# Performance work log

Measured on AMD Instinct MI355X. Metric: run time of the kernel, lower is better.

## Reference

```python
import jax, jax.numpy as jnp
import numpy as np

T, B, D_IN, H, N_OUT = 512, 256, 85, 512, 33

def setup_inputs() -> dict:
    key = jax.random.key(0)
    ks = jax.random.split(key, 16)
    s_in = 1.0 / np.sqrt(D_IN)
    s_h = 1.0 / np.sqrt(H)
    def u(k, shape, s):
        return jax.random.uniform(k, shape, jnp.float32, -s, s)
    return {
        "x": jax.random.normal(ks[0], (T, B, D_IN), jnp.float32),
        "Wxi": u(ks[1], (H, D_IN), s_in),
        "Wxf": u(ks[2], (H, D_IN), s_in),
        "Wxo": u(ks[3], (H, D_IN), s_in),
        "Wxc": u(ks[4], (H, D_IN), s_in),
        "Whi": u(ks[5], (H, H), s_h), "bhi": u(ks[6], (H,), s_h),
        "Whf": u(ks[7], (H, H), s_h), "bhf": u(ks[8], (H,), s_h),
        "Who": u(ks[9], (H, H), s_h), "bho": u(ks[10], (H,), s_h),
        "Whc": u(ks[11], (H, H), s_h), "bhc": u(ks[12], (H,), s_h),
        "Wro": u(ks[13], (N_OUT, H), s_h), "bro": u(ks[14], (N_OUT,), s_h),
    }

def _lstm(x, Wxi, Wxf, Wxo, Wxc, Whi, bhi, Whf, bhf, Who, bho, Whc, bhc, Wro, bro):
    act = jnp.tanh  # hp['activation'] == 'tanh'
    # Precompute all input-side projections in one big GEMM-like pass: [T,B,H]
    xi = jnp.einsum('tbi,hi->tbh', x, Wxi)
    xf = jnp.einsum('tbi,hi->tbh', x, Wxf)
    xo = jnp.einsum('tbi,hi->tbh', x, Wxo)
    xc = jnp.einsum('tbi,hi->tbh', x, Wxc)
    Bsz = x.shape[1]
    Hd = Whi.shape[0]
    C0 = jnp.zeros((Bsz, Hd), x.dtype)
    H0 = jnp.zeros((Bsz, Hd), x.dtype)

    def step(carry, xs):
        C, Hs = carry
        xi_t, xf_t, xo_t, xc_t = xs
        I = jax.nn.sigmoid(xi_t + Hs @ Whi.T + bhi)
        F = jax.nn.sigmoid(xf_t + Hs @ Whf.T + bhf)
        O = jax.nn.sigmoid(xo_t + Hs @ Who.T + bho)
        C_hat = act(xc_t + Hs @ Whc.T + bhc)
        C = F * C + I * C_hat
        Hs = O * act(C)
        return (C, Hs), Hs

    _, hidden_states = jax.lax.scan(step, (C0, H0), (xi, xf, xo, xc))
    # readout over all timesteps: [T,B,n_output]
    return jnp.einsum('tbh,oh->tbo', hidden_states, Wro) + bro

def reference(x, Wxi, Wxf, Wxo, Wxc, Whi, bhi, Whf, bhf, Who, bho, Whc, bhc, Wro, bro):
    return _lstm(x, Wxi, Wxf, Wxo, Wxc, Whi, bhi, Whf, bhf, Who, bho, Whc, bhc, Wro, bro)
```

## Files before the change

### kernel.cpp

```cpp
#include <hip/hip_runtime.h>
#include <hip/hip_bf16.h>
#include <stdint.h>

#define T_STEPS 512
#define BATCH   256
#define DIN     85
#define HDIM    512
#define NOUT    33

#define GRP   16
#define BBLK  16
#define HS    32
#define LDA   1040
#define LDX   208

#define SENT  0x7FC07FC0u

typedef __attribute__((ext_vector_type(8))) short s8v;
typedef __attribute__((ext_vector_type(4))) float f4v;
typedef __attribute__((ext_vector_type(4))) uint32_t u32x4;

__device__ __forceinline__ uint16_t f2bf(float f) {
    uint32_t x = __builtin_bit_cast(uint32_t, f);
    uint32_t r = (x + 0x7fffu + ((x >> 16) & 1u)) >> 16;
    return (uint16_t)r;
}
__device__ __forceinline__ float sigm(float v) {
    v = fminf(fmaxf(v, -30.f), 30.f);
    return 1.f / (1.f + __expf(-v));
}
__device__ __forceinline__ float tanh_f(float v) {
    v = fminf(fmaxf(v, -15.f), 15.f);
    float e = __expf(2.f * v);
    return (e - 1.f) / (e + 1.f);
}
__device__ __forceinline__ s8v cvt8(const float* p) {
    s8v v;
#pragma unroll
    for (int j = 0; j < 8; ++j) v[j] = (short)f2bf(p[j]);
    return v;
}

__device__ __forceinline__ void issue4(u32x4& v, const uint32_t* p) {
    asm volatile("global_load_dwordx4 %0, %1, off sc0 sc1"
                 : "+v"(v) : "v"(p) : "memory");
}
__device__ __forceinline__ void wait_vm1(u32x4& a, u32x4& b, u32x4& c, u32x4& d) {
    asm volatile("s_waitcnt vmcnt(1)"
                 : "+v"(a), "+v"(b), "+v"(c), "+v"(d) :: "memory");
}
__device__ __forceinline__ void wait_vm0(u32x4& a, u32x4& b, u32x4& c, u32x4& d) {
    asm volatile("s_waitcnt vmcnt(0)"
                 : "+v"(a), "+v"(b), "+v"(c), "+v"(d) :: "memory");
}
__device__ __forceinline__ uint32_t has_sent(const u32x4& v) {
    return (uint32_t)(v[0] == SENT) | (uint32_t)(v[1] == SENT) |
           (uint32_t)(v[2] == SENT) | (uint32_t)(v[3] == SENT);
}

__global__ __launch_bounds__(256) void lstm_init(uint32_t* __restrict__ hbuf)
{
    const size_t n4 = (size_t)(T_STEPS + 1) * BATCH * HDIM / 2 / 4;
    u32x4 s; s[0] = SENT; s[1] = SENT; s[2] = SENT; s[3] = SENT;
    u32x4* p = (u32x4*)hbuf;
    for (size_t i = (size_t)blockIdx.x * 256 + threadIdx.x; i < n4;
         i += (size_t)gridDim.x * 256)
        p[i] = s;
}

__global__ __launch_bounds__(256, 1) void lstm_rec(
    const float* __restrict__ x,
    const float* __restrict__ Wxi, const float* __restrict__ Wxf,
    const float* __restrict__ Wxo, const float* __restrict__ Wxc,
    const float* __restrict__ Whi, const float* __restrict__ bhi,
    const float* __restrict__ Whf, const float* __restrict__ bhf,
    const float* __restrict__ Who, const float* __restrict__ bho,
    const float* __restrict__ Whc, const float* __restrict__ bhc,
    uint16_t* __restrict__ hbuf)
{
    __shared__ __align__(16) uint8_t hA[16 * LDA];
    __shared__ __align__(16) uint8_t xA[16 * LDX];
    __shared__ float gbuf[4 * 16 * 33];

    const int tid  = threadIdx.x;
    const int bid  = blockIdx.x;
    const int xcd  = bid & 7;
    const int slot = bid >> 3;
    const int grp  = xcd * 2 + (slot >> 4);
    const int mem  = slot & 15;
    const int b0   = grp * BBLK;
    const int hs   = mem * HS;

    const int wave  = tid >> 6;
    const int lane  = tid & 63;
    const int col16 = lane & 15;
    const int quad  = lane >> 4;

    const float* Wh  = (wave == 0) ? Whi : (wave == 1) ? Whf : (wave == 2) ? Who : Whc;
    const float* Wxp = (wave == 0) ? Wxi : (wave == 1) ? Wxf : (wave == 2) ? Wxo : Wxc;

    s8v bh[2][16];
#pragma unroll
    for (int nt = 0; nt < 2; ++nt) {
        const float* rowp = Wh + (size_t)(hs + nt * 16 + col16) * HDIM;
#pragma unroll
        for (int kt = 0; kt < 16; ++kt)
            bh[nt][kt] = cvt8(rowp + kt * 32 + quad * 8);
    }
    s8v bx[2][3];
#pragma unroll
    for (int nt = 0; nt < 2; ++nt) {
        const float* rowp = Wxp + (size_t)(hs + nt * 16 + col16) * DIN;
#pragma unroll
        for (int kt = 0; kt < 3; ++kt) {
            s8v v;
#pragma unroll
            for (int j = 0; j < 8; ++j) {
                int k = kt * 32 + quad * 8 + j;
                v[j] = (k < DIN) ? (short)f2bf(rowp[k]) : (short)0;
            }
            bx[nt][kt] = v;
        }
    }

    const int r  = tid >> 4;
    const int c0 = (tid & 15) * 2;
    const float bi0 = bhi[hs + c0], bi1 = bhi[hs + c0 + 1];
    const float bf0 = bhf[hs + c0], bf1 = bhf[hs + c0 + 1];
    const float bo0 = bho[hs + c0], bo1 = bho[hs + c0 + 1];
    const float bc0 = bhc[hs + c0], bc1 = bhc[hs + c0 + 1];
    float C0 = 0.f, C1 = 0.f;

    uint32_t* hbuf32 = (uint32_t*)hbuf;
    const size_t hslot = ((size_t)(b0 + r) * HDIM + hs + c0) >> 1;

    const int rrow[4] = { tid >> 6, (tid + 256) >> 6, (tid + 512) >> 6, (tid + 768) >> 6 };
    const int rc8     = tid & 63;

    float xreg[6];
    auto load_x = [&](int t) {
#pragma unroll
        for (int j = 0; j < 6; ++j) {
            int v = tid + j * 256;
            int row = v / 96, k = v % 96;
            xreg[j] = (k < DIN) ? x[(size_t)(t * BATCH + b0 + row) * DIN + k] : 0.f;
        }
    };
    auto store_x = [&]() {
#pragma unroll
        for (int j = 0; j < 6; ++j) {
            int v = tid + j * 256;
            int row = v / 96, k = v % 96;
            *(uint16_t*)(xA + row * LDX + k * 2) = f2bf(xreg[j]);
        }
    };

    load_x(0);
    for (int j = tid; j < 16 * LDA / 16; j += 256) {
        s8v z;
#pragma unroll
        for (int q = 0; q < 8; ++q) z[q] = 0;
        ((s8v*)hA)[j] = z;
    }
    store_x();
    __syncthreads();

    u32x4 v0 = {SENT, SENT, SENT, SENT};
    u32x4 v1 = v0, v2 = v0, v3 = v0;

    for (int t = 0; t < T_STEPS; ++t) {
        const int last = (t == T_STEPS - 1);

        if (!last) load_x(t + 1);

        f4v acc0 = {0.f, 0.f, 0.f, 0.f}, acc1 = {0.f, 0.f, 0.f, 0.f};
#pragma unroll
        for (int kt = 0; kt < 16; ++kt) {
            s8v a = *(const s8v*)(hA + col16 * LDA + kt * 64 + quad * 16);
            acc0 = __builtin_amdgcn_mfma_f32_16x16x32_bf16(a, bh[0][kt], acc0, 0, 0, 0);
            acc1 = __builtin_amdgcn_mfma_f32_16x16x32_bf16(a, bh[1][kt], acc1, 0, 0, 0);
        }
#pragma unroll
        for (int kt = 0; kt < 3; ++kt) {
            s8v a = *(const s8v*)(xA + col16 * LDX + kt * 64 + quad * 16);
            acc0 = __builtin_amdgcn_mfma_f32_16x16x32_bf16(a, bx[0][kt], acc0, 0, 0, 0);
            acc1 = __builtin_amdgcn_mfma_f32_16x16x32_bf16(a, bx[1][kt], acc1, 0, 0, 0);
        }
#pragma unroll
        for (int rr = 0; rr < 4; ++rr) {
            int b = quad * 4 + rr;
            gbuf[(wave * 16 + b) * 33 + col16]      = acc0[rr];
            gbuf[(wave * 16 + b) * 33 + 16 + col16] = acc1[rr];
        }

        __syncthreads();

        const uint32_t* src = hbuf32 + (size_t)(t + 1) * (BATCH * HDIM / 2)
                                     + (size_t)b0 * (HDIM / 2);
        const uint32_t* p0 = src + (size_t)rrow[0] * (HDIM / 2) + rc8 * 4;
        const uint32_t* p1 = src + (size_t)rrow[1] * (HDIM / 2) + rc8 * 4;
        const uint32_t* p2 = src + (size_t)rrow[2] * (HDIM / 2) + rc8 * 4;
        const uint32_t* p3 = src + (size_t)rrow[3] * (HDIM / 2) + rc8 * 4;
        if (!last) {
            issue4(v0, p0); issue4(v1, p1); issue4(v2, p2); issue4(v3, p3);
            store_x();
        }

        float pi0 = gbuf[(0 * 16 + r) * 33 + c0] + bi0;
        float pi1 = gbuf[(0 * 16 + r) * 33 + c0 + 1] + bi1;
        float pf0 = gbuf[(1 * 16 + r) * 33 + c0] + bf0;
        float pf1 = gbuf[(1 * 16 + r) * 33 + c0 + 1] + bf1;
        float po0 = gbuf[(2 * 16 + r) * 33 + c0] + bo0;
        float po1 = gbuf[(2 * 16 + r) * 33 + c0 + 1] + bo1;
        float pc0 = gbuf[(3 * 16 + r) * 33 + c0] + bc0;
        float pc1 = gbuf[(3 * 16 + r) * 33 + c0 + 1] + bc1;

        float I0 = sigm(pi0), F0 = sigm(pf0), O0 = sigm(po0), G0 = tanh_f(pc0);
        float I1 = sigm(pi1), F1 = sigm(pf1), O1 = sigm(po1), G1 = tanh_f(pc1);
        C0 = F0 * C0 + I0 * G0;
        C1 = F1 * C1 + I1 * G1;
        float h0 = O0 * tanh_f(C0);
        float h1 = O1 * tanh_f(C1);

        uint32_t packed = (uint32_t)f2bf(h0) | ((uint32_t)f2bf(h1) << 16);
        __hip_atomic_store(&hbuf32[(size_t)(t + 1) * (BATCH * HDIM / 2) + hslot],
                           packed, __ATOMIC_RELAXED, __HIP_MEMORY_SCOPE_AGENT);

        if (last) break;

        wait_vm1(v0, v1, v2, v3);
        uint32_t s0 = has_sent(v0), s1 = has_sent(v1),
                 s2 = has_sent(v2), s3 = has_sent(v3);
        int round = 0;
        while (s0 | s1 | s2 | s3) {
            if (++round > 50000) break;
            if (round >= 6) __builtin_amdgcn_s_sleep(2);
            if (s0) issue4(v0, p0);
            if (s1) issue4(v1, p1);
            if (s2) issue4(v2, p2);
            if (s3) issue4(v3, p3);
            wait_vm0(v0, v1, v2, v3);
            s0 = has_sent(v0); s1 = has_sent(v1);
            s2 = has_sent(v2); s3 = has_sent(v3);
        }
        *(u32x4*)(hA + rrow[0] * LDA + rc8 * 16) = v0;
        *(u32x4*)(hA + rrow[1] * LDA + rc8 * 16) = v1;
        *(u32x4*)(hA + rrow[2] * LDA + rc8 * 16) = v2;
        *(u32x4*)(hA + rrow[3] * LDA + rc8 * 16) = v3;

        __syncthreads();
    }
}

__global__ __launch_bounds__(256, 1) void lstm_out(
    const uint16_t* __restrict__ hbuf,
    const float* __restrict__ Wro, const float* __restrict__ bro,
    float* __restrict__ out)
{
    __shared__ __align__(16) uint8_t hT[64 * LDA];

    const int tid   = threadIdx.x;
    const int bid   = blockIdx.x;
    const int wave  = tid >> 6;
    const int lane  = tid & 63;
    const int col16 = lane & 15;
    const int quad  = lane >> 4;

    s8v bw[3][16];
    float bias[3];
#pragma unroll
    for (int nt = 0; nt < 3; ++nt) {
        int o = nt * 16 + col16;
        bias[nt] = (o < NOUT) ? bro[o] : 0.f;
#pragma unroll
        for (int kt = 0; kt < 16; ++kt) {
            if (o < NOUT) {
                bw[nt][kt] = cvt8(Wro + (size_t)o * HDIM + kt * 32 + quad * 8);
            } else {
                s8v z;
#pragma unroll
                for (int q = 0; q < 8; ++q) z[q] = 0;
                bw[nt][kt] = z;
            }
        }
    }

    const uint16_t* hsrc = hbuf + (size_t)BATCH * HDIM;

    for (int sub = 0; sub < 8; ++sub) {
        size_t row0 = (size_t)bid * 512 + (size_t)sub * 64;
#pragma unroll
        for (int j = 0; j < 16; ++j) {
            int v = tid + j * 256;
            int row = v >> 6, c8 = v & 63;
            s8v val = *(const s8v*)(hsrc + (row0 + row) * HDIM + c8 * 8);
            *(s8v*)(hT + row * LDA + c8 * 16) = val;
        }
        __syncthreads();

        f4v acc[3];
#pragma unroll
        for (int nt = 0; nt < 3; ++nt) acc[nt] = (f4v){0.f, 0.f, 0.f, 0.f};
#pragma unroll
        for (int kt = 0; kt < 16; ++kt) {
            s8v a = *(const s8v*)(hT + (wave * 16 + col16) * LDA + kt * 64 + quad * 16);
#pragma unroll
            for (int nt = 0; nt < 3; ++nt)
                acc[nt] = __builtin_amdgcn_mfma_f32_16x16x32_bf16(a, bw[nt][kt], acc[nt], 0, 0, 0);
        }
#pragma unroll
        for (int nt = 0; nt < 3; ++nt) {
            int o = nt * 16 + col16;
            if (o < NOUT) {
#pragma unroll
                for (int rr = 0; rr < 4; ++rr) {
                    size_t rg = row0 + (size_t)wave * 16 + quad * 4 + rr;
                    out[rg * NOUT + o] = acc[nt][rr] + bias[nt];
                }
            }
        }
        __syncthreads();
    }
}

extern "C" void kernel_launch(void* const* d_in, const int* in_sizes, int n_in,
                              void* d_out, int out_size, void* d_ws, size_t ws_size,
                              hipStream_t stream)
{
    const float* x   = (const float*)d_in[0];
    const float* Wxi = (const float*)d_in[1];
    const float* Wxf = (const float*)d_in[2];
    const float* Wxo = (const float*)d_in[3];
    const float* Wxc = (const float*)d_in[4];
    const float* Whi = (const float*)d_in[5];
    const float* bhi = (const float*)d_in[6];
    const float* Whf = (const float*)d_in[7];
    const float* bhf = (const float*)d_in[8];
    const float* Who = (const float*)d_in[9];
    const float* bho = (const float*)d_in[10];
    const float* Whc = (const float*)d_in[11];
    const float* bhc = (const float*)d_in[12];
    const float* Wro = (const float*)d_in[13];
    const float* bro = (const float*)d_in[14];
    float* out = (float*)d_out;

    uint16_t* hbuf = (uint16_t*)d_ws;

    lstm_init<<<2048, 256, 0, stream>>>((uint32_t*)hbuf);
    lstm_rec<<<256, 256, 0, stream>>>(x, Wxi, Wxf, Wxo, Wxc,
                                      Whi, bhi, Whf, bhf, Who, bho, Whc, bhc,
                                      hbuf);
    lstm_out<<<256, 256, 0, stream>>>(hbuf, Wro, bro, out);
}
```

Before: 1.339 ms.

## Move gate activations into MFMA waves and skip re-reading own h slice

Each gate wave now adds its bias and applies sigmoid or tanh in registers before writing to shared memory, so the cell-update threads only read finished gate values. Threads write their own packed h directly into the local LDS tile and skip the global poll for the columns this block produced. The global loads for the next h are now issued after the local h is computed instead of being overlapped with the gate math. This trims polling traffic and per-step latency on the serial recurrence, but it gives up the earlier overlap between the in-flight global loads and the activation math.

```diff
diff --git a/kernel.cpp b/kernel.cpp
--- a/kernel.cpp
+++ b/kernel.cpp
@@ -8,7 +8,6 @@
 #define HDIM    512
 #define NOUT    33
 
-#define GRP   16
 #define BBLK  16
 #define HS    32
 #define LDA   1040
@@ -41,13 +40,9 @@
     return v;
 }
 
-__device__ __forceinline__ void issue4(u32x4& v, const uint32_t* p) {
+__device__ __forceinline__ void issue4_dev(u32x4& v, const uint32_t* p) {
     asm volatile("global_load_dwordx4 %0, %1, off sc0 sc1"
                  : "+v"(v) : "v"(p) : "memory");
-}
-__device__ __forceinline__ void wait_vm1(u32x4& a, u32x4& b, u32x4& c, u32x4& d) {
-    asm volatile("s_waitcnt vmcnt(1)"
-                 : "+v"(a), "+v"(b), "+v"(c), "+v"(d) :: "memory");
 }
 __device__ __forceinline__ void wait_vm0(u32x4& a, u32x4& b, u32x4& c, u32x4& d) {
     asm volatile("s_waitcnt vmcnt(0)"
@@ -98,6 +93,7 @@
 
     const float* Wh  = (wave == 0) ? Whi : (wave == 1) ? Whf : (wave == 2) ? Who : Whc;
     const float* Wxp = (wave == 0) ? Wxi : (wave == 1) ? Wxf : (wave == 2) ? Wxo : Wxc;
+    const float* bg  = (wave == 0) ? bhi : (wave == 1) ? bhf : (wave == 2) ? bho : bhc;
 
     s8v bh[2][16];
 #pragma unroll
@@ -122,13 +118,11 @@
             bx[nt][kt] = v;
         }
     }
+    const float bg0 = bg[hs + col16];
+    const float bg1 = bg[hs + 16 + col16];
 
     const int r  = tid >> 4;
     const int c0 = (tid & 15) * 2;
-    const float bi0 = bhi[hs + c0], bi1 = bhi[hs + c0 + 1];
-    const float bf0 = bhf[hs + c0], bf1 = bhf[hs + c0 + 1];
-    const float bo0 = bho[hs + c0], bo1 = bho[hs + c0 + 1];
-    const float bc0 = bhc[hs + c0], bc1 = bhc[hs + c0 + 1];
     float C0 = 0.f, C1 = 0.f;
 
     uint32_t* hbuf32 = (uint32_t*)hbuf;
@@ -136,6 +130,7 @@
 
     const int rrow[4] = { tid >> 6, (tid + 256) >> 6, (tid + 512) >> 6, (tid + 768) >> 6 };
     const int rc8     = tid & 63;
+    const uint32_t ownm = (rc8 >= mem * 4 && rc8 < mem * 4 + 4) ? 1u : 0u;
 
     float xreg[6];
     auto load_x = [&](int t) {
@@ -188,12 +183,35 @@
         }
 #pragma unroll
         for (int rr = 0; rr < 4; ++rr) {
+            float a0 = acc0[rr] + bg0;
+            float a1 = acc1[rr] + bg1;
+            if (wave == 3) { a0 = tanh_f(a0); a1 = tanh_f(a1); }
+            else           { a0 = sigm(a0);   a1 = sigm(a1);   }
             int b = quad * 4 + rr;
-            gbuf[(wave * 16 + b) * 33 + col16]      = acc0[rr];
-            gbuf[(wave * 16 + b) * 33 + 16 + col16] = acc1[rr];
+            gbuf[(wave * 16 + b) * 33 + col16]      = a0;
+            gbuf[(wave * 16 + b) * 33 + 16 + col16] = a1;
         }
 
         __syncthreads();
+
+        if (!last) store_x();
+
+        float I0 = gbuf[(0 * 16 + r) * 33 + c0], I1 = gbuf[(0 * 16 + r) * 33 + c0 + 1];
+        float F0 = gbuf[(1 * 16 + r) * 33 + c0], F1 = gbuf[(1 * 16 + r) * 33 + c0 + 1];
+        float O0 = gbuf[(2 * 16 + r) * 33 + c0], O1 = gbuf[(2 * 16 + r) * 33 + c0 + 1];
+        float G0 = gbuf[(3 * 16 + r) * 33 + c0], G1 = gbuf[(3 * 16 + r) * 33 + c0 + 1];
+        C0 = F0 * C0 + I0 * G0;
+        C1 = F1 * C1 + I1 * G1;
+        float h0 = O0 * tanh_f(C0);
+        float h1 = O1 * tanh_f(C1);
+
+        uint32_t packed = (uint32_t)f2bf(h0) | ((uint32_t)f2bf(h1) << 16);
+        __hip_atomic_store(&hbuf32[(size_t)(t + 1) * (BATCH * HDIM / 2) + hslot],
+                           packed, __ATOMIC_RELAXED, __HIP_MEMORY_SCOPE_AGENT);
+
+        if (last) break;
+
+        *(uint32_t*)(hA + r * LDA + (hs + c0) * 2) = packed;
 
         const uint32_t* src = hbuf32 + (size_t)(t + 1) * (BATCH * HDIM / 2)
                                      + (size_t)b0 * (HDIM / 2);
@@ -201,52 +219,34 @@
         const uint32_t* p1 = src + (size_t)rrow[1] * (HDIM / 2) + rc8 * 4;
         const uint32_t* p2 = src + (size_t)rrow[2] * (HDIM / 2) + rc8 * 4;
         const uint32_t* p3 = src + (size_t)rrow[3] * (HDIM / 2) + rc8 * 4;
-        if (!last) {
-            issue4(v0, p0); issue4(v1, p1); issue4(v2, p2); issue4(v3, p3);
-            store_x();
-        }
-
-        float pi0 = gbuf[(0 * 16 + r) * 33 + c0] + bi0;
-        float pi1 = gbuf[(0 * 16 + r) * 33 + c0 + 1] + bi1;
-        float pf0 = gbuf[(1 * 16 + r) * 33 + c0] + bf0;
-        float pf1 = gbuf[(1 * 16 + r) * 33 + c0 + 1] + bf1;
-        float po0 = gbuf[(2 * 16 + r) * 33 + c0] + bo0;
-        float po1 = gbuf[(2 * 16 + r) * 33 + c0 + 1] + bo1;
-        float pc0 = gbuf[(3 * 16 + r) * 33 + c0] + bc0;
-        float pc1 = gbuf[(3 * 16 + r) * 33 + c0 + 1] + bc1;
-
-        float I0 = sigm(pi0), F0 = sigm(pf0), O0 = sigm(po0), G0 = tanh_f(pc0);
-        float I1 = sigm(pi1), F1 = sigm(pf1), O1 = sigm(po1), G1 = tanh_f(pc1);
-        C0 = F0 * C0 + I0 * G0;
-        C1 = F1 * C1 + I1 * G1;
-        float h0 = O0 * tanh_f(C0);
-        float h1 = O1 * tanh_f(C1);
-
-        uint32_t packed = (uint32_t)f2bf(h0) | ((uint32_t)f2bf(h1) << 16);
-        __hip_atomic_store(&hbuf32[(size_t)(t + 1) * (BATCH * HDIM / 2) + hslot],
-                           packed, __ATOMIC_RELAXED, __HIP_MEMORY_SCOPE_AGENT);
-
-        if (last) break;
-
-        wait_vm1(v0, v1, v2, v3);
-        uint32_t s0 = has_sent(v0), s1 = has_sent(v1),
-                 s2 = has_sent(v2), s3 = has_sent(v3);
+
+        if (!ownm) {
+            issue4_dev(v0, p0); issue4_dev(v1, p1);
+            issue4_dev(v2, p2); issue4_dev(v3, p3);
+        }
+        wait_vm0(v0, v1, v2, v3);
+        uint32_t s0 = ownm ? 0u : has_sent(v0);
+        uint32_t s1 = ownm ? 0u : has_sent(v1);
+        uint32_t s2 = ownm ? 0u : has_sent(v2);
+        uint32_t s3 = ownm ? 0u : has_sent(v3);
         int round = 0;
         while (s0 | s1 | s2 | s3) {
             if (++round > 50000) break;
-            if (round >= 6) __builtin_amdgcn_s_sleep(2);
-            if (s0) issue4(v0, p0);
-            if (s1) issue4(v1, p1);
-            if (s2) issue4(v2, p2);
-            if (s3) issue4(v3, p3);
+            if (round >= 8) __builtin_amdgcn_s_sleep(1);
+            if (s0) issue4_dev(v0, p0);
+            if (s1) issue4_dev(v1, p1);
+            if (s2) issue4_dev(v2, p2);
+            if (s3) issue4_dev(v3, p3);
             wait_vm0(v0, v1, v2, v3);
             s0 = has_sent(v0); s1 = has_sent(v1);
             s2 = has_sent(v2); s3 = has_sent(v3);
         }
-        *(u32x4*)(hA + rrow[0] * LDA + rc8 * 16) = v0;
-        *(u32x4*)(hA + rrow[1] * LDA + rc8 * 16) = v1;
-        *(u32x4*)(hA + rrow[2] * LDA + rc8 * 16) = v2;
-        *(u32x4*)(hA + rrow[3] * LDA + rc8 * 16) = v3;
+        if (!ownm) {
+            *(u32x4*)(hA + rrow[0] * LDA + rc8 * 16) = v0;
+            *(u32x4*)(hA + rrow[1] * LDA + rc8 * 16) = v1;
+            *(u32x4*)(hA + rrow[2] * LDA + rc8 * 16) = v2;
+            *(u32x4*)(hA + rrow[3] * LDA + rc8 * 16) = v3;
+        }
 
         __syncthreads();
     }
```

Result: slower. 1.704 ms (+27.3%).
